# Kernel optimization log

Measured on AMD Instinct MI355X. Metric: run time of the kernel, lower is better.

## Reference

```python
import jax, jax.numpy as jnp
import numpy as np

INPUT_DIMS = 32
OUTPUT_DIMS = 1024
SEQ_LEN = 1024
BATCH = 64


def positional_encoding(max_len, d_model):
    pos = np.arange(max_len)[:, None].astype(np.float64)      # [L,1]
    i = np.arange(d_model)[None, :].astype(np.float64)        # [1,D]
    even_i = i - (i % 2)                                      # i for even, i-1 for odd
    angle = pos / np.power(10000.0, even_i / d_model)         # [L,D]
    pe = np.where(i % 2 == 0, np.sin(angle), np.cos(angle))
    return jnp.asarray(pe, dtype=jnp.float32)


def activation_quant(x):
    # per-token absmax int8 quant (BitNet b1.58)
    scale = 127.0 / jnp.clip(jnp.max(jnp.abs(x), axis=-1, keepdims=True), 1e-5, None)
    return jnp.clip(jnp.round(x * scale), -128, 127) / scale


def weight_quant(w):
    # per-tensor ternary quant via mean absmax
    scale = 1.0 / jnp.clip(jnp.mean(jnp.abs(w)), 1e-5, None)
    return jnp.clip(jnp.round(w * scale), -1, 1) / scale


def setup_inputs() -> dict:
    key = jax.random.key(0)
    k1, k2, k3 = jax.random.split(key, 3)
    x = jax.random.normal(k1, (BATCH, SEQ_LEN, INPUT_DIMS), dtype=jnp.float32)
    bound = 1.0 / np.sqrt(INPUT_DIMS)
    W = jax.random.uniform(k2, (OUTPUT_DIMS, INPUT_DIMS), minval=-bound, maxval=bound, dtype=jnp.float32)
    b = jax.random.uniform(k3, (OUTPUT_DIMS,), minval=-bound, maxval=bound, dtype=jnp.float32)
    return {"x": x, "W": W, "b": b}


def reference(x, W, b):
    # BitLinear with straight-through estimator
    x_eff = x + jax.lax.stop_gradient(activation_quant(x) - x)
    w_eff = W + jax.lax.stop_gradient(weight_quant(W) - W)
    emb = jnp.einsum('bsk,ok->bso', x_eff, w_eff) + b  # [B,S,O]
    pe = positional_encoding(SEQ_LEN, OUTPUT_DIMS)     # [L,O]
    return emb + pe[: emb.shape[-2]]
```

## Files before the change

kernel.cpp:

```cpp
#include <hip/hip_runtime.h>
#include <cstdint>
#include <cstddef>

#define BATCH   64
#define SEQLEN  1024
#define KDIM    32
#define ODIM    1024
#define NTOK    (BATCH * SEQLEN)

#define NWP 8
#define NQX 1024

typedef __attribute__((ext_vector_type(8))) short bf16x8;
typedef __attribute__((ext_vector_type(4))) float f32x4;

__device__ __forceinline__ unsigned short f32_to_bf16_exact(float f) {
    union { float f; unsigned int u; } cv; cv.f = f;
    return (unsigned short)(cv.u >> 16);
}

__global__ __launch_bounds__(256) void prep_kernel(const float* __restrict__ x,
                                                   const float* __restrict__ W,
                                                   float* __restrict__ partial,
                                                   unsigned short* __restrict__ xq,
                                                   float* __restrict__ rxs) {
    const int blk = blockIdx.x;
    const int t   = threadIdx.x;

    if (blk < NWP) {
        __shared__ float red[256];
        const float4* W4 = reinterpret_cast<const float4*>(W) + (size_t)blk * 1024 + t * 4;
        float acc = 0.f;
        #pragma unroll
        for (int j = 0; j < 4; ++j) {
            float4 v = W4[j];
            acc += fabsf(v.x) + fabsf(v.y) + fabsf(v.z) + fabsf(v.w);
        }
        red[t] = acc;
        __syncthreads();
        for (int step = 128; step > 0; step >>= 1) {
            if (t < step) red[t] += red[t + step];
            __syncthreads();
        }
        if (t == 0) partial[blk] = red[0];
    } else {
        const int g = (blk - NWP) * 256 + t;
        const float* xg = x + ((size_t)g << 3);
        float4 xa = *reinterpret_cast<const float4*>(xg);
        float4 xb = *reinterpret_cast<const float4*>(xg + 4);
        float a = fmaxf(fmaxf(fmaxf(fabsf(xa.x), fabsf(xa.y)),
                              fmaxf(fabsf(xa.z), fabsf(xa.w))),
                        fmaxf(fmaxf(fabsf(xb.x), fabsf(xb.y)),
                              fmaxf(fabsf(xb.z), fabsf(xb.w))));
        a = fmaxf(a, __shfl_xor(a, 1, 4));
        a = fmaxf(a, __shfl_xor(a, 2, 4));
        const float am = fmaxf(a, 1e-5f);
        const float scale = 127.0f / am;
        float e[8] = {xa.x, xa.y, xa.z, xa.w, xb.x, xb.y, xb.z, xb.w};
        union { bf16x8 v; unsigned short s[8]; } u;
        #pragma unroll
        for (int j = 0; j < 8; ++j)
            u.s[j] = f32_to_bf16_exact(rintf(e[j] * scale));
        *reinterpret_cast<bf16x8*>(xq + ((size_t)g << 3)) = u.v;
        if ((g & 3) == 0) rxs[g >> 2] = am * (1.0f / 127.0f);
    }
}

__global__ __launch_bounds__(512) void bitgemm(
    const unsigned short* __restrict__ xq,
    const float*          __restrict__ rxs,
    const float*          __restrict__ W,
    const float*          __restrict__ partial,
    const float*          __restrict__ bias,
    float* __restrict__ out)
{
    const int lane = threadIdx.x & 63;
    const int wid  = threadIdx.x >> 6;
    const int l15  = lane & 15;
    const int hi   = lane >> 4;

    const int lb    = (blockIdx.x & 7) * 64 + (blockIdx.x >> 3);
    const int sblk  = lb >> 3;
    const int oblk  = lb & 3;
    const int bhalf = (lb >> 2) & 1;
    const int o0    = oblk * 256 + (wid & 3) * 64;
    const int s0    = sblk * 16;
    const int bq    = bhalf * 2 + (wid >> 2);

    float tot = 0.f;
    #pragma unroll
    for (int p = 0; p < 8; ++p) tot += partial[p];
    const float rw = fmaxf(tot * (1.0f / 32768.0f), 1e-5f);
    const float sc = 1.0f / rw;

    bf16x8 afrag[4];
    #pragma unroll
    for (int f = 0; f < 4; ++f) {
        const float* wr = W + (size_t)(o0 + f * 16 + l15) * KDIM + hi * 8;
        float4 wa = *reinterpret_cast<const float4*>(wr);
        float4 wb = *reinterpret_cast<const float4*>(wr + 4);
        float e[8] = {wa.x, wa.y, wa.z, wa.w, wb.x, wb.y, wb.z, wb.w};
        union { bf16x8 v; unsigned short s[8]; } u;
        #pragma unroll
        for (int j = 0; j < 8; ++j)
            u.s[j] = f32_to_bf16_exact(fminf(fmaxf(rintf(e[j] * sc), -1.0f), 1.0f));
        afrag[f] = u.v;
    }

    const float C  = -0.012976281620653759f;
    const float sf = (float)(s0 + l15);
    f32x4 addf[4];
    #pragma unroll
    for (int f = 0; f < 4; ++f) {
        const int oe = o0 + f * 16 + hi * 4;
        f32x4 bv = *reinterpret_cast<const f32x4*>(bias + oe);
        float a0 = sf * exp2f(C * (float)oe);
        float a1 = sf * exp2f(C * (float)(oe + 2));
        addf[f][0] = bv[0] + sinf(a0);
        addf[f][1] = bv[1] + cosf(a0);
        addf[f][2] = bv[2] + sinf(a1);
        addf[f][3] = bv[3] + cosf(a1);
    }

    #pragma unroll 2
    for (int i = 0; i < 16; ++i) {
        const int b   = bq * 16 + i;
        const int tok = (b << 10) + s0 + l15;

        bf16x8 bfrag = *reinterpret_cast<const bf16x8*>(
            xq + ((size_t)tok << 5) + hi * 8);
        const float rxw = rxs[tok] * rw;

        float* op = out + ((size_t)tok << 10) + o0 + hi * 4;
        #pragma unroll
        for (int f = 0; f < 4; ++f) {
            f32x4 acc = (f32x4){0.f, 0.f, 0.f, 0.f};
            acc = __builtin_amdgcn_mfma_f32_16x16x32_bf16(afrag[f], bfrag, acc, 0, 0, 0);
            f32x4 r;
            #pragma unroll
            for (int j = 0; j < 4; ++j)
                r[j] = fmaf(acc[j], rxw, addf[f][j]);
            *reinterpret_cast<f32x4*>(op + f * 16) = r;
        }
    }
}

extern "C" void kernel_launch(void* const* d_in, const int* in_sizes, int n_in,
                              void* d_out, int out_size, void* d_ws, size_t ws_size,
                              hipStream_t stream) {
    const float* x = (const float*)d_in[0];
    const float* W = (const float*)d_in[1];
    const float* b = (const float*)d_in[2];
    float* out = (float*)d_out;

    char* wsb = (char*)d_ws;
    float*          partial = (float*)wsb;
    float*          rxs     = (float*)(wsb + 256);
    unsigned short* xq      = (unsigned short*)(wsb + (512u << 10));

    prep_kernel<<<NWP + NQX, 256, 0, stream>>>(x, W, partial, xq, rxs);
    bitgemm<<<512, 512, 0, stream>>>(xq, rxs, W, partial, b, out);
}
```

Measured before the change: 57.29 us.

## Fuse weight and activation quantization into the GEMM kernel as one launch

Removes the separate prep kernel and has each GEMM block reduce the full weight abs-sum itself and quantize activations on the fly from fp32 x, using cross-lane shuffles to form the per-token absmax. This removes one kernel launch and the workspace round trip for quantized activations and scales. In exchange, every block re-reads all of W (128 KB) and redundantly quantizes x tokens that other output-blocks also use. Launch bounds also ask for 4 blocks per CU.

Result: slower. 85.49 us (+49.2%).

```diff
diff --git a/kernel.cpp b/kernel.cpp
--- a/kernel.cpp
+++ b/kernel.cpp
@@ -8,9 +8,6 @@
 #define ODIM    1024
 #define NTOK    (BATCH * SEQLEN)
 
-#define NWP 8
-#define NQX 1024
-
 typedef __attribute__((ext_vector_type(8))) short bf16x8;
 typedef __attribute__((ext_vector_type(4))) float f32x4;
 
@@ -19,63 +16,17 @@
     return (unsigned short)(cv.u >> 16);
 }
 
-__global__ __launch_bounds__(256) void prep_kernel(const float* __restrict__ x,
-                                                   const float* __restrict__ W,
-                                                   float* __restrict__ partial,
-                                                   unsigned short* __restrict__ xq,
-                                                   float* __restrict__ rxs) {
-    const int blk = blockIdx.x;
-    const int t   = threadIdx.x;
-
-    if (blk < NWP) {
-        __shared__ float red[256];
-        const float4* W4 = reinterpret_cast<const float4*>(W) + (size_t)blk * 1024 + t * 4;
-        float acc = 0.f;
-        #pragma unroll
-        for (int j = 0; j < 4; ++j) {
-            float4 v = W4[j];
-            acc += fabsf(v.x) + fabsf(v.y) + fabsf(v.z) + fabsf(v.w);
-        }
-        red[t] = acc;
-        __syncthreads();
-        for (int step = 128; step > 0; step >>= 1) {
-            if (t < step) red[t] += red[t + step];
-            __syncthreads();
-        }
-        if (t == 0) partial[blk] = red[0];
-    } else {
-        const int g = (blk - NWP) * 256 + t;
-        const float* xg = x + ((size_t)g << 3);
-        float4 xa = *reinterpret_cast<const float4*>(xg);
-        float4 xb = *reinterpret_cast<const float4*>(xg + 4);
-        float a = fmaxf(fmaxf(fmaxf(fabsf(xa.x), fabsf(xa.y)),
-                              fmaxf(fabsf(xa.z), fabsf(xa.w))),
-                        fmaxf(fmaxf(fabsf(xb.x), fabsf(xb.y)),
-                              fmaxf(fabsf(xb.z), fabsf(xb.w))));
-        a = fmaxf(a, __shfl_xor(a, 1, 4));
-        a = fmaxf(a, __shfl_xor(a, 2, 4));
-        const float am = fmaxf(a, 1e-5f);
-        const float scale = 127.0f / am;
-        float e[8] = {xa.x, xa.y, xa.z, xa.w, xb.x, xb.y, xb.z, xb.w};
-        union { bf16x8 v; unsigned short s[8]; } u;
-        #pragma unroll
-        for (int j = 0; j < 8; ++j)
-            u.s[j] = f32_to_bf16_exact(rintf(e[j] * scale));
-        *reinterpret_cast<bf16x8*>(xq + ((size_t)g << 3)) = u.v;
-        if ((g & 3) == 0) rxs[g >> 2] = am * (1.0f / 127.0f);
-    }
-}
-
-__global__ __launch_bounds__(512) void bitgemm(
-    const unsigned short* __restrict__ xq,
-    const float*          __restrict__ rxs,
-    const float*          __restrict__ W,
-    const float*          __restrict__ partial,
-    const float*          __restrict__ bias,
+__global__ __launch_bounds__(512, 4) void bitgemm_mono(
+    const float* __restrict__ x,
+    const float* __restrict__ W,
+    const float* __restrict__ bias,
     float* __restrict__ out)
 {
-    const int lane = threadIdx.x & 63;
-    const int wid  = threadIdx.x >> 6;
+    __shared__ float red[512];
+
+    const int t    = threadIdx.x;
+    const int lane = t & 63;
+    const int wid  = t >> 6;
     const int l15  = lane & 15;
     const int hi   = lane >> 4;
 
@@ -87,10 +38,22 @@
     const int s0    = sblk * 16;
     const int bq    = bhalf * 2 + (wid >> 2);
 
-    float tot = 0.f;
-    #pragma unroll
-    for (int p = 0; p < 8; ++p) tot += partial[p];
-    const float rw = fmaxf(tot * (1.0f / 32768.0f), 1e-5f);
+    {
+        const float4* W4 = reinterpret_cast<const float4*>(W) + (size_t)t * 16;
+        float acc = 0.f;
+        #pragma unroll
+        for (int j = 0; j < 16; ++j) {
+            float4 v = W4[j];
+            acc += fabsf(v.x) + fabsf(v.y) + fabsf(v.z) + fabsf(v.w);
+        }
+        red[t] = acc;
+        __syncthreads();
+        for (int step = 256; step > 0; step >>= 1) {
+            if (t < step) red[t] += red[t + step];
+            __syncthreads();
+        }
+    }
+    const float rw = fmaxf(red[0] * (1.0f / 32768.0f), 1e-5f);
     const float sc = 1.0f / rw;
 
     bf16x8 afrag[4];
@@ -127,15 +90,32 @@
         const int b   = bq * 16 + i;
         const int tok = (b << 10) + s0 + l15;
 
-        bf16x8 bfrag = *reinterpret_cast<const bf16x8*>(
-            xq + ((size_t)tok << 5) + hi * 8);
-        const float rxw = rxs[tok] * rw;
+        const float* xr = x + ((size_t)tok << 5) + hi * 8;
+        float4 xa = *reinterpret_cast<const float4*>(xr);
+        float4 xb = *reinterpret_cast<const float4*>(xr + 4);
+
+        float am = fmaxf(fmaxf(fmaxf(fabsf(xa.x), fabsf(xa.y)),
+                               fmaxf(fabsf(xa.z), fabsf(xa.w))),
+                         fmaxf(fmaxf(fabsf(xb.x), fabsf(xb.y)),
+                               fmaxf(fabsf(xb.z), fabsf(xb.w))));
+        am = fmaxf(am, __shfl_xor(am, 16));
+        am = fmaxf(am, __shfl_xor(am, 32));
+        am = fmaxf(am, 1e-5f);
+        const float xscale = 127.0f / am;
+        union { bf16x8 v; unsigned short s[8]; } bu;
+        {
+            float e[8] = {xa.x, xa.y, xa.z, xa.w, xb.x, xb.y, xb.z, xb.w};
+            #pragma unroll
+            for (int j = 0; j < 8; ++j)
+                bu.s[j] = f32_to_bf16_exact(rintf(e[j] * xscale));
+        }
+        const float rxw = am * (1.0f / 127.0f) * rw;
 
         float* op = out + ((size_t)tok << 10) + o0 + hi * 4;
         #pragma unroll
         for (int f = 0; f < 4; ++f) {
             f32x4 acc = (f32x4){0.f, 0.f, 0.f, 0.f};
-            acc = __builtin_amdgcn_mfma_f32_16x16x32_bf16(afrag[f], bfrag, acc, 0, 0, 0);
+            acc = __builtin_amdgcn_mfma_f32_16x16x32_bf16(afrag[f], bu.v, acc, 0, 0, 0);
             f32x4 r;
             #pragma unroll
             for (int j = 0; j < 4; ++j)
@@ -153,11 +133,5 @@
     const float* b = (const float*)d_in[2];
     float* out = (float*)d_out;
 
-    char* wsb = (char*)d_ws;
-    float*          partial = (float*)wsb;
-    float*          rxs     = (float*)(wsb + 256);
-    unsigned short* xq      = (unsigned short*)(wsb + (512u << 10));
-
-    prep_kernel<<<NWP + NQX, 256, 0, stream>>>(x, W, partial, xq, rxs);
-    bitgemm<<<512, 512, 0, stream>>>(xq, rxs, W, partial, b, out);
+    bitgemm_mono<<<512, 512, 0, stream>>>(x, W, b, out);
 }
```
